# Kernel tuning notes

Hardware: AMD Instinct MI355X
Metric: run time of the kernel (lower is better)

## Reference

```python
import jax, jax.numpy as jnp
import numpy as np
from jax import lax

K = 3
STRIDE = 1
PAD = 1
DIL = 1


def setup_inputs() -> dict:
    key = jax.random.key(0)
    k1, k2, k3 = jax.random.split(key, 3)
    B, C, H, W = 8, 128, 64, 64
    O = 128
    x = jax.random.normal(k1, (B, C, H, W), jnp.float32)
    # offset-predicting conv weights (small init -> small offsets, as in DCN practice)
    w_off = jax.random.normal(k2, (2 * K * K, C, K, K), jnp.float32) * 0.01
    b_off = jnp.zeros((2 * K * K,), jnp.float32)
    # deformable conv weight [O, Cin, K, K], bias=False in the source
    w = jax.random.normal(k3, (O, C, K, K), jnp.float32) * (1.0 / np.sqrt(C * K * K))
    return {"x": x, "w_off": w_off, "b_off": b_off, "w": w}


def _deform_conv(x, offset, w):
    # x: [B,C,H,W]; offset: [B, 2*K*K, Ho, Wo]; w: [O,C,K,K]
    B, C, H, W = x.shape
    Ho, Wo = offset.shape[2], offset.shape[3]
    K2 = K * K
    off = offset.reshape(B, K2, 2, Ho, Wo)
    oy, ox = off[:, :, 0], off[:, :, 1]            # [B,K2,Ho,Wo]
    ky = (jnp.arange(K2) // K).astype(jnp.float32)  # kernel row per tap
    kx = (jnp.arange(K2) % K).astype(jnp.float32)
    base_y = (jnp.arange(Ho) * STRIDE - PAD).astype(jnp.float32)
    base_x = (jnp.arange(Wo) * STRIDE - PAD).astype(jnp.float32)
    py = base_y[None, None, :, None] + ky[None, :, None, None] * DIL + oy
    px = base_x[None, None, None, :] + kx[None, :, None, None] * DIL + ox

    y0 = jnp.floor(py)
    x0 = jnp.floor(px)
    dy = py - y0
    dx = px - x0
    y0i = y0.astype(jnp.int32)
    x0i = x0.astype(jnp.int32)
    bidx = jnp.arange(B)[:, None, None, None]

    def gather(yi, xi):
        valid = (yi >= 0) & (yi < H) & (xi >= 0) & (xi < W)
        yc = jnp.clip(yi, 0, H - 1)
        xc = jnp.clip(xi, 0, W - 1)
        v = x[bidx, :, yc, xc]  # [B,K2,Ho,Wo,C]
        return v * valid[..., None]

    v00 = gather(y0i, x0i)
    v01 = gather(y0i, x0i + 1)
    v10 = gather(y0i + 1, x0i)
    v11 = gather(y0i + 1, x0i + 1)
    samp = (v00 * ((1 - dy) * (1 - dx))[..., None]
            + v01 * ((1 - dy) * dx)[..., None]
            + v10 * (dy * (1 - dx))[..., None]
            + v11 * (dy * dx)[..., None])  # [B,K2,Ho,Wo,C]

    O = w.shape[0]
    return jnp.einsum('bkhwc,ock->bohw', samp, w.reshape(O, C, K2))


def reference(x, w_off, b_off, w):
    # offset conv: standard conv2d, stride/pad/dilation as in __init__
    offset = lax.conv_general_dilated(
        x, w_off, window_strides=(STRIDE, STRIDE),
        padding=[(PAD, PAD), (PAD, PAD)], rhs_dilation=(DIL, DIL))
    offset = offset + b_off[None, :, None, None]
    return _deform_conv(x, offset, w)
```

## Files before the change

kernel.cpp:

```cpp
#include <hip/hip_runtime.h>

#define B_ 8
#define C_ 128
#define H_ 64
#define W_ 64
#define O_ 128
#define F_ 18
#define K2_ 9
#define HW_ 4096
#define CK2_ 1152

#define WR_ 10
#define WC_ 22

typedef __attribute__((ext_vector_type(8))) short short8_t;
typedef __attribute__((ext_vector_type(4))) float f32x4_t;
typedef __attribute__((ext_vector_type(4))) unsigned int uint4_t;

__device__ inline short bf16r(float f) {
  unsigned u = __builtin_bit_cast(unsigned, f);
  u += 0x7FFFu + ((u >> 16) & 1u);
  return (short)(u >> 16);
}
__device__ inline float bflo(unsigned u) {
  return __builtin_bit_cast(float, u << 16);
}
__device__ inline float bfhi(unsigned u) {
  return __builtin_bit_cast(float, u & 0xFFFF0000u);
}

__global__ __launch_bounds__(256) void prep_all_kernel(
    const float* __restrict__ w, const float* __restrict__ w_off,
    const float* __restrict__ x,
    short* __restrict__ w_bt2, short* __restrict__ w_ot2,
    short* __restrict__ x_t) {
  __shared__ float tile[128][65];
  int bid = blockIdx.x, t = threadIdx.x;
  if (bid < 576) {
    int i = bid * 256 + t;
    int kk2 = i & 31, o = (i >> 5) & 127, ks = i >> 12;
    w_bt2[i] = bf16r(w[(o * C_ + (ks & 3) * 32 + kk2) * K2_ + (ks >> 2)]);
  } else if (bid < 720) {
    int i = (bid - 576) * 256 + t;
    int kk2 = i & 31, f = (i >> 5) & 31, ks = i >> 10;
    w_ot2[i] = (f < F_) ? bf16r(w_off[(f * C_ + (ks & 3) * 32 + kk2) * K2_ + (ks >> 2)])
                        : (short)0;
  } else {
    int xb_id = bid - 720;
    int b = xb_id >> 6;
    int p_base = (xb_id & 63) << 6;
    const float* xb = x + ((long)b << 19);
#pragma unroll
    for (int i = 0; i < 32; ++i) {
      int idx = (i << 8) + t;
      int c = idx >> 6, p = idx & 63;
      tile[c][p] = xb[((long)c << 12) + p_base + p];
    }
    __syncthreads();
#pragma unroll
    for (int i = 0; i < 32; ++i) {
      int idx = (i << 8) + t;
      int p = idx >> 7, c = idx & 127;
      x_t[(((long)(b << 12) + p_base + p) << 7) + c] = bf16r(tile[c][p]);
    }
  }
}

__device__ inline short8_t lds16(const short* xs, int pix, int ch) {
  return *(const short8_t*)(xs + (pix << 7) + ((ch ^ (pix & 7)) << 3));
}

__global__ __launch_bounds__(512, 4) void fused_deform_kernel(
    const short* __restrict__ x_t, const short* __restrict__ w_ot2,
    const float* __restrict__ b_off, const short* __restrict__ w_bt2,
    float* __restrict__ out) {
  __shared__ short xs[WR_ * WC_ * 128];
  __shared__ float offs[4][16][20];

  int tid = threadIdx.x;
  int wv = tid >> 6, lane = tid & 63;
  int row = wv & 3, g = wv >> 2;
  int fr = lane & 15, q = lane >> 4;
  int bid = (int)blockIdx.x;
  int b = bid & 7;
  int tile_id = bid >> 3;
  int ho0 = (tile_id >> 2) << 2;
  int x0b = (tile_id & 3) << 4;
  int ys  = min(max(ho0 - 3, 0), H_ - WR_);
  int xsL = min(max(x0b - 3, 0), W_ - WC_);
  int ye2 = ys + WR_ - 1, xe2 = xsL + WC_ - 1;

  const short* xtb = x_t + ((long)b << 19);

#pragma unroll
  for (int i = 0; i < 7; ++i) {
    int ci = (i << 9) + tid;
    if (ci < WR_ * WC_ * 16) {
      int pix = ci >> 4, ch = ci & 15;
      int yr = pix / WC_, xr = pix - yr * WC_;
      short8_t v = *(const short8_t*)(xtb + ((((ys + yr) << 6) + xsL + xr) << 7) + (ch << 3));
      *(short8_t*)(xs + (pix << 7) + ((ch ^ (pix & 7)) << 3)) = v;
    }
  }
  __syncthreads();

  int ho = ho0 + row;
  int wo = x0b + fr;

  {
    f32x4_t oacc0 = (f32x4_t){0.f, 0.f, 0.f, 0.f};
    f32x4_t oacc1 = (f32x4_t){0.f, 0.f, 0.f, 0.f};
#pragma unroll
    for (int kt = 0; kt < 9; ++kt) {
      int y = ho + kt / 3 - 1, xx = wo + kt % 3 - 1;
      bool ok = (y >= 0) & (y < H_) & (xx >= 0) & (xx < W_);
      int yc = min(max(y, 0), H_ - 1), xc = min(max(xx, 0), W_ - 1);
      int pixA = (yc - ys) * WC_ + (xc - xsL);
#pragma unroll
      for (int sh = 0; sh < 2; ++sh) {
        int s = (g << 1) | sh;
        short8_t bfv = lds16(xs, pixA, (s << 2) + q);
        if (!ok) bfv = (short8_t){0, 0, 0, 0, 0, 0, 0, 0};
        int ks = (kt << 2) + s;
        short8_t a0 = *(const short8_t*)(w_ot2 + (((ks << 5) + fr) << 5) + (q << 3));
        short8_t a1 = *(const short8_t*)(w_ot2 + (((ks << 5) + 16 + fr) << 5) + (q << 3));
        oacc0 = __builtin_amdgcn_mfma_f32_16x16x32_bf16(a0, bfv, oacc0, 0, 0, 0);
        oacc1 = __builtin_amdgcn_mfma_f32_16x16x32_bf16(a1, bfv, oacc1, 0, 0, 0);
      }
    }
    if (g == 0) {
#pragma unroll
      for (int r = 0; r < 4; ++r) {
        int f0 = (q << 2) + r;
        offs[row][fr][f0] = oacc0[r] + b_off[f0];
      }
      if (q == 0) {
        offs[row][fr][16] = oacc1[0] + b_off[16];
        offs[row][fr][17] = oacc1[1] + b_off[17];
      }
    }
    __syncthreads();
    if (g == 1) {
#pragma unroll
      for (int r = 0; r < 4; ++r) {
        int f0 = (q << 2) + r;
        offs[row][fr][f0] += oacc0[r];
      }
      if (q == 0) {
        offs[row][fr][16] += oacc1[0];
        offs[row][fr][17] += oacc1[1];
      }
    }
  }
  __syncthreads();

  f32x4_t acc[8];
#pragma unroll
  for (int nf = 0; nf < 8; ++nf) acc[nf] = (f32x4_t){0.f, 0.f, 0.f, 0.f};

#pragma unroll
  for (int kt = 0; kt < 9; ++kt) {
    float oy = offs[row][fr][2 * kt];
    float ox = offs[row][fr][2 * kt + 1];

    float py = (float)(ho + kt / 3 - 1) + oy;
    float px = (float)(wo + kt % 3 - 1) + ox;
    float fy0 = floorf(py), fx0 = floorf(px);
    float dy = py - fy0, dx = px - fx0;
    int y0 = (int)fy0, x0 = (int)fx0;
    int y1 = y0 + 1, x1 = x0 + 1;
    float my0 = (y0 >= 0 && y0 < H_) ? 1.f : 0.f;
    float my1 = (y1 >= 0 && y1 < H_) ? 1.f : 0.f;
    float mx0 = (x0 >= 0 && x0 < W_) ? 1.f : 0.f;
    float mx1 = (x1 >= 0 && x1 < W_) ? 1.f : 0.f;
    float w00 = (1.f - dy) * (1.f - dx) * my0 * mx0;
    float w01 = (1.f - dy) * dx * my0 * mx1;
    float w10 = dy * (1.f - dx) * my1 * mx0;
    float w11 = dy * dx * my1 * mx1;
    int y0c = min(max(y0, 0), H_ - 1), y1c = min(max(y1, 0), H_ - 1);
    int x0c = min(max(x0, 0), W_ - 1), x1c = min(max(x1, 0), W_ - 1);
    int p00 = (y0c - ys) * WC_ + (x0c - xsL), p01 = p00 + (x1c - x0c);
    int p10 = (y1c - ys) * WC_ + (x0c - xsL), p11 = p10 + (x1c - x0c);

    short8_t v00[2], v01[2], v10[2], v11[2];
    unsigned long long bad =
        __ballot((y0c < ys) || (y1c > ye2) || (x0c < xsL) || (x1c > xe2));
    if (bad == 0ULL) {
#pragma unroll
      for (int sh = 0; sh < 2; ++sh) {
        int s = (g << 1) | sh;
        int ch = (s << 2) + q;
        v00[sh] = lds16(xs, p00, ch);
        v01[sh] = lds16(xs, p01, ch);
        v10[sh] = lds16(xs, p10, ch);
        v11[sh] = lds16(xs, p11, ch);
      }
    } else {
      const short* g00 = xtb + (((y0c << 6) + x0c) << 7);
      const short* g01 = xtb + (((y0c << 6) + x1c) << 7);
      const short* g10 = xtb + (((y1c << 6) + x0c) << 7);
      const short* g11 = xtb + (((y1c << 6) + x1c) << 7);
#pragma unroll
      for (int sh = 0; sh < 2; ++sh) {
        int s = (g << 1) | sh;
        int c0 = (s << 5) + (q << 3);
        v00[sh] = *(const short8_t*)(g00 + c0);
        v01[sh] = *(const short8_t*)(g01 + c0);
        v10[sh] = *(const short8_t*)(g10 + c0);
        v11[sh] = *(const short8_t*)(g11 + c0);
      }
    }

#pragma unroll
    for (int sh = 0; sh < 2; ++sh) {
      int s = (g << 1) | sh;
      uint4_t u00 = __builtin_bit_cast(uint4_t, v00[sh]);
      uint4_t u01 = __builtin_bit_cast(uint4_t, v01[sh]);
      uint4_t u10 = __builtin_bit_cast(uint4_t, v10[sh]);
      uint4_t u11 = __builtin_bit_cast(uint4_t, v11[sh]);
      uint4_t sfu;
#pragma unroll
      for (int d = 0; d < 4; ++d) {
        float rlo = w00 * bflo(u00[d]) + w01 * bflo(u01[d]) +
                    w10 * bflo(u10[d]) + w11 * bflo(u11[d]);
        float rhi = w00 * bfhi(u00[d]) + w01 * bfhi(u01[d]) +
                    w10 * bfhi(u10[d]) + w11 * bfhi(u11[d]);
        unsigned p;
        asm("v_cvt_pk_bf16_f32 %0, %1, %2" : "=v"(p) : "v"(rlo), "v"(rhi));
        sfu[d] = p;
      }
      short8_t sf = __builtin_bit_cast(short8_t, sfu);
      int ks = (kt << 2) + s;
      const short* wp = w_bt2 + (((ks << 7) + fr) << 5) + (q << 3);
#pragma unroll
      for (int nf = 0; nf < 8; ++nf) {
        short8_t wf = *(const short8_t*)(wp + (nf << 9));
        acc[nf] = __builtin_amdgcn_mfma_f32_16x16x32_bf16(wf, sf, acc[nf], 0, 0, 0);
      }
    }
  }

  __syncthreads();
  float* red = (float*)xs;
  if (g == 1) {
#pragma unroll
    for (int nf = 0; nf < 8; ++nf) {
      *(f32x4_t*)&red[(row * 16 + fr) * 136 + (nf << 4) + (q << 2)] = acc[nf];
    }
  }
  __syncthreads();
  if (g == 0) {
    float* ob = out + ((long)(b * O_) << 12) + (ho << 6) + wo;
#pragma unroll
    for (int nf = 0; nf < 8; ++nf) {
      f32x4_t other = *(const f32x4_t*)&red[(row * 16 + fr) * 136 + (nf << 4) + (q << 2)];
#pragma unroll
      for (int r = 0; r < 4; ++r) {
        ob[(long)((nf << 4) + (q << 2) + r) << 12] = acc[nf][r] + other[r];
      }
    }
  }
}

extern "C" void kernel_launch(void* const* d_in, const int* in_sizes, int n_in,
                              void* d_out, int out_size, void* d_ws, size_t ws_size,
                              hipStream_t stream) {
  const float* x     = (const float*)d_in[0];
  const float* w_off = (const float*)d_in[1];
  const float* b_off = (const float*)d_in[2];
  const float* w     = (const float*)d_in[3];
  float* out = (float*)d_out;

  short* w_bt2 = (short*)d_ws;
  short* w_ot2 = (short*)((char*)d_ws + 294912);
  short* x_t   = (short*)((char*)d_ws + 294912 + 73728);

  prep_all_kernel<<<1232, 256, 0, stream>>>(w, w_off, x, w_bt2, w_ot2, x_t);
  fused_deform_kernel<<<512, 512, 0, stream>>>(x_t, w_ot2, b_off, w_bt2, out);
}
```

Before: 60.07 us.

## Halve output rows per block and split channels across four wave groups

```diff
diff --git a/kernel.cpp b/kernel.cpp
--- a/kernel.cpp
+++ b/kernel.cpp
@@ -10,7 +10,7 @@
 #define HW_ 4096
 #define CK2_ 1152
 
-#define WR_ 10
+#define WR_ 8
 #define WC_ 22
 
 typedef __attribute__((ext_vector_type(8))) short short8_t;
@@ -70,21 +70,21 @@
   return *(const short8_t*)(xs + (pix << 7) + ((ch ^ (pix & 7)) << 3));
 }
 
-__global__ __launch_bounds__(512, 4) void fused_deform_kernel(
+__global__ __launch_bounds__(512, 6) void fused_deform_kernel(
     const short* __restrict__ x_t, const short* __restrict__ w_ot2,
     const float* __restrict__ b_off, const short* __restrict__ w_bt2,
     float* __restrict__ out) {
   __shared__ short xs[WR_ * WC_ * 128];
-  __shared__ float offs[4][16][20];
+  __shared__ float offs[2][16][20];
 
   int tid = threadIdx.x;
   int wv = tid >> 6, lane = tid & 63;
-  int row = wv & 3, g = wv >> 2;
+  int row = wv & 1, g = wv >> 1;
   int fr = lane & 15, q = lane >> 4;
   int bid = (int)blockIdx.x;
   int b = bid & 7;
   int tile_id = bid >> 3;
-  int ho0 = (tile_id >> 2) << 2;
+  int ho0 = (tile_id >> 2) << 1;
   int x0b = (tile_id & 3) << 4;
   int ys  = min(max(ho0 - 3, 0), H_ - WR_);
   int xsL = min(max(x0b - 3, 0), W_ - WC_);
@@ -93,7 +93,7 @@
   const short* xtb = x_t + ((long)b << 19);
 
 #pragma unroll
-  for (int i = 0; i < 7; ++i) {
+  for (int i = 0; i < 6; ++i) {
     int ci = (i << 9) + tid;
     if (ci < WR_ * WC_ * 16) {
       int pix = ci >> 4, ch = ci & 15;
@@ -116,17 +116,13 @@
       bool ok = (y >= 0) & (y < H_) & (xx >= 0) & (xx < W_);
       int yc = min(max(y, 0), H_ - 1), xc = min(max(xx, 0), W_ - 1);
       int pixA = (yc - ys) * WC_ + (xc - xsL);
-#pragma unroll
-      for (int sh = 0; sh < 2; ++sh) {
-        int s = (g << 1) | sh;
-        short8_t bfv = lds16(xs, pixA, (s << 2) + q);
-        if (!ok) bfv = (short8_t){0, 0, 0, 0, 0, 0, 0, 0};
-        int ks = (kt << 2) + s;
-        short8_t a0 = *(const short8_t*)(w_ot2 + (((ks << 5) + fr) << 5) + (q << 3));
-        short8_t a1 = *(const short8_t*)(w_ot2 + (((ks << 5) + 16 + fr) << 5) + (q << 3));
-        oacc0 = __builtin_amdgcn_mfma_f32_16x16x32_bf16(a0, bfv, oacc0, 0, 0, 0);
-        oacc1 = __builtin_amdgcn_mfma_f32_16x16x32_bf16(a1, bfv, oacc1, 0, 0, 0);
-      }
+      short8_t bfv = lds16(xs, pixA, (g << 2) + q);
+      if (!ok) bfv = (short8_t){0, 0, 0, 0, 0, 0, 0, 0};
+      int ks = (kt << 2) + g;
+      short8_t a0 = *(const short8_t*)(w_ot2 + (((ks << 5) + fr) << 5) + (q << 3));
+      short8_t a1 = *(const short8_t*)(w_ot2 + (((ks << 5) + 16 + fr) << 5) + (q << 3));
+      oacc0 = __builtin_amdgcn_mfma_f32_16x16x32_bf16(a0, bfv, oacc0, 0, 0, 0);
+      oacc1 = __builtin_amdgcn_mfma_f32_16x16x32_bf16(a1, bfv, oacc1, 0, 0, 0);
     }
     if (g == 0) {
 #pragma unroll
@@ -140,19 +136,22 @@
       }
     }
     __syncthreads();
-    if (g == 1) {
-#pragma unroll
-      for (int r = 0; r < 4; ++r) {
-        int f0 = (q << 2) + r;
-        offs[row][fr][f0] += oacc0[r];
-      }
-      if (q == 0) {
-        offs[row][fr][16] += oacc1[0];
-        offs[row][fr][17] += oacc1[1];
-      }
-    }
-  }
-  __syncthreads();
+#pragma unroll
+    for (int gs = 1; gs < 4; ++gs) {
+      if (g == gs) {
+#pragma unroll
+        for (int r = 0; r < 4; ++r) {
+          int f0 = (q << 2) + r;
+          offs[row][fr][f0] += oacc0[r];
+        }
+        if (q == 0) {
+          offs[row][fr][16] += oacc1[0];
+          offs[row][fr][17] += oacc1[1];
+        }
+      }
+      __syncthreads();
+    }
+  }
 
   f32x4_t acc[8];
 #pragma unroll
@@ -182,81 +181,80 @@
     int p00 = (y0c - ys) * WC_ + (x0c - xsL), p01 = p00 + (x1c - x0c);
     int p10 = (y1c - ys) * WC_ + (x0c - xsL), p11 = p10 + (x1c - x0c);
 
-    short8_t v00[2], v01[2], v10[2], v11[2];
+    short8_t v00, v01, v10, v11;
     unsigned long long bad =
         __ballot((y0c < ys) || (y1c > ye2) || (x0c < xsL) || (x1c > xe2));
     if (bad == 0ULL) {
-#pragma unroll
-      for (int sh = 0; sh < 2; ++sh) {
-        int s = (g << 1) | sh;
-        int ch = (s << 2) + q;
-        v00[sh] = lds16(xs, p00, ch);
-        v01[sh] = lds16(xs, p01, ch);
-        v10[sh] = lds16(xs, p10, ch);
-        v11[sh] = lds16(xs, p11, ch);
-      }
+      int ch = (g << 2) + q;
+      v00 = lds16(xs, p00, ch);
+      v01 = lds16(xs, p01, ch);
+      v10 = lds16(xs, p10, ch);
+      v11 = lds16(xs, p11, ch);
     } else {
-      const short* g00 = xtb + (((y0c << 6) + x0c) << 7);
-      const short* g01 = xtb + (((y0c << 6) + x1c) << 7);
-      const short* g10 = xtb + (((y1c << 6) + x0c) << 7);
-      const short* g11 = xtb + (((y1c << 6) + x1c) << 7);
-#pragma unroll
-      for (int sh = 0; sh < 2; ++sh) {
-        int s = (g << 1) | sh;
-        int c0 = (s << 5) + (q << 3);
-        v00[sh] = *(const short8_t*)(g00 + c0);
-        v01[sh] = *(const short8_t*)(g01 + c0);
-        v10[sh] = *(const short8_t*)(g10 + c0);
-        v11[sh] = *(const short8_t*)(g11 + c0);
-      }
-    }
-
-#pragma unroll
-    for (int sh = 0; sh < 2; ++sh) {
-      int s = (g << 1) | sh;
-      uint4_t u00 = __builtin_bit_cast(uint4_t, v00[sh]);
-      uint4_t u01 = __builtin_bit_cast(uint4_t, v01[sh]);
-      uint4_t u10 = __builtin_bit_cast(uint4_t, v10[sh]);
-      uint4_t u11 = __builtin_bit_cast(uint4_t, v11[sh]);
-      uint4_t sfu;
-#pragma unroll
-      for (int d = 0; d < 4; ++d) {
-        float rlo = w00 * bflo(u00[d]) + w01 * bflo(u01[d]) +
-                    w10 * bflo(u10[d]) + w11 * bflo(u11[d]);
-        float rhi = w00 * bfhi(u00[d]) + w01 * bfhi(u01[d]) +
-                    w10 * bfhi(u10[d]) + w11 * bfhi(u11[d]);
-        unsigned p;
-        asm("v_cvt_pk_bf16_f32 %0, %1, %2" : "=v"(p) : "v"(rlo), "v"(rhi));
-        sfu[d] = p;
-      }
-      short8_t sf = __builtin_bit_cast(short8_t, sfu);
-      int ks = (kt << 2) + s;
-      const short* wp = w_bt2 + (((ks << 7) + fr) << 5) + (q << 3);
-#pragma unroll
-      for (int nf = 0; nf < 8; ++nf) {
-        short8_t wf = *(const short8_t*)(wp + (nf << 9));
-        acc[nf] = __builtin_amdgcn_mfma_f32_16x16x32_bf16(wf, sf, acc[nf], 0, 0, 0);
-      }
+      int c0 = (g << 5) + (q << 3);
+      v00 = *(const short8_t*)(xtb + (((y0c << 6) + x0c) << 7) + c0);
+      v01 = *(const short8_t*)(xtb + (((y0c << 6) + x1c) << 7) + c0);
+      v10 = *(const short8_t*)(xtb + (((y1c << 6) + x0c) << 7) + c0);
+      v11 = *(const short8_t*)(xtb + (((y1c << 6) + x1c) << 7) + c0);
+    }
+
+    uint4_t u00 = __builtin_bit_cast(uint4_t, v00);
+    uint4_t u01 = __builtin_bit_cast(uint4_t, v01);
+    uint4_t u10 = __builtin_bit_cast(uint4_t, v10);
+    uint4_t u11 = __builtin_bit_cast(uint4_t, v11);
+    uint4_t sfu;
+#pragma unroll
+    for (int d = 0; d < 4; ++d) {
+      float rlo = w00 * bflo(u00[d]) + w01 * bflo(u01[d]) +
+                  w10 * bflo(u10[d]) + w11 * bflo(u11[d]);
+      float rhi = w00 * bfhi(u00[d]) + w01 * bfhi(u01[d]) +
+                  w10 * bfhi(u10[d]) + w11 * bfhi(u11[d]);
+      unsigned p;
+      asm("v_cvt_pk_bf16_f32 %0, %1, %2" : "=v"(p) : "v"(rlo), "v"(rhi));
+      sfu[d] = p;
+    }
+    short8_t sf = __builtin_bit_cast(short8_t, sfu);
+    int ks = (kt << 2) + g;
+    const short* wp = w_bt2 + (((ks << 7) + fr) << 5) + (q << 3);
+#pragma unroll
+    for (int nf = 0; nf < 8; ++nf) {
+      short8_t wf = *(const short8_t*)(wp + (nf << 9));
+      acc[nf] = __builtin_amdgcn_mfma_f32_16x16x32_bf16(wf, sf, acc[nf], 0, 0, 0);
     }
   }
 
   __syncthreads();
   float* red = (float*)xs;
-  if (g == 1) {
+  int ri = (row * 16 + fr) * 132 + (q << 2);
+  if (g == 1 || g == 3) {
+    float* z = red + (g >> 1) * 4224;
+#pragma unroll
+    for (int nf = 0; nf < 8; ++nf) *(f32x4_t*)&z[ri + (nf << 4)] = acc[nf];
+  }
+  __syncthreads();
+  if (g == 0 || g == 2) {
+    const float* z = red + (g >> 1) * 4224;
 #pragma unroll
     for (int nf = 0; nf < 8; ++nf) {
-      *(f32x4_t*)&red[(row * 16 + fr) * 136 + (nf << 4) + (q << 2)] = acc[nf];
-    }
+      f32x4_t o4 = *(const f32x4_t*)&z[ri + (nf << 4)];
+#pragma unroll
+      for (int r = 0; r < 4; ++r) acc[nf][r] += o4[r];
+    }
+  }
+  __syncthreads();
+  if (g == 2) {
+#pragma unroll
+    for (int nf = 0; nf < 8; ++nf) *(f32x4_t*)&red[ri + (nf << 4)] = acc[nf];
   }
   __syncthreads();
   if (g == 0) {
     float* ob = out + ((long)(b * O_) << 12) + (ho << 6) + wo;
 #pragma unroll
     for (int nf = 0; nf < 8; ++nf) {
-      f32x4_t other = *(const f32x4_t*)&red[(row * 16 + fr) * 136 + (nf << 4) + (q << 2)];
+      f32x4_t o4 = *(const f32x4_t*)&red[ri + (nf << 4)];
 #pragma unroll
       for (int r = 0; r < 4; ++r) {
-        ob[(long)((nf << 4) + (q << 2) + r) << 12] = acc[nf][r] + other[r];
+        ob[(long)((nf << 4) + (q << 2) + r) << 12] = acc[nf][r] + o4[r];
       }
     }
   }
@@ -276,5 +274,5 @@
   short* x_t   = (short*)((char*)d_ws + 294912 + 73728);
 
   prep_all_kernel<<<1232, 256, 0, stream>>>(w, w_off, x, w_bt2, w_ot2, x_t);
-  fused_deform_kernel<<<512, 512, 0, stream>>>(x_t, w_ot2, b_off, w_bt2, out);
-}
+  fused_deform_kernel<<<1024, 512, 0, stream>>>(x_t, w_ot2, b_off, w_bt2, out);
+}
```

Measured after the change: 61.27 us. 2.0% more time.
